# Kernel tuning notes

Hardware: AMD Instinct MI355X
Metric: run time of the kernel (lower is better)

The kernel has to match this reference:

```python
import math
import jax, jax.numpy as jnp
import numpy as np

LAMBDA_INIT = 0.8
GN_EPS = 1e-5

B, H, S, D = 2, 16, 2048, 128  # batch, heads, seq, head_dim


def setup_inputs() -> dict:
    key = jax.random.key(0)
    ks = jax.random.split(key, 8)
    return {
        "q": jax.random.normal(ks[0], (B, H, S, 2 * D), dtype=jnp.float32),
        "k": jax.random.normal(ks[1], (B, H, S, 2 * D), dtype=jnp.float32),
        "v": jax.random.normal(ks[2], (B, H, S, D), dtype=jnp.float32),
        "lam_q1": jax.random.normal(ks[3], (D,), dtype=jnp.float32),
        "lam_q2": jax.random.normal(ks[4], (D,), dtype=jnp.float32),
        "lam_k1": jax.random.normal(ks[5], (D,), dtype=jnp.float32),
        "lam_k2": jax.random.normal(ks[6], (D,), dtype=jnp.float32),
        "gn_weight": jnp.ones((H * D,), dtype=jnp.float32),
        "gn_bias": jnp.zeros((H * D,), dtype=jnp.float32),
    }


def reference(q, k, v, lam_q1, lam_q2, lam_k1, lam_k2, gn_weight, gn_bias):
    d = q.shape[-1] // 2
    scale = 1.0 / math.sqrt(d)
    Q1, Q2 = q[..., :d], q[..., d:]
    K1, K2 = k[..., :d], k[..., d:]
    # dual score matrices [B,H,S,S]
    w1 = jax.nn.softmax(jnp.einsum('bhsd,bhtd->bhst', Q1, K1) * scale, axis=-1)
    w2 = jax.nn.softmax(jnp.einsum('bhsd,bhtd->bhst', Q2, K2) * scale, axis=-1)
    lam = jnp.exp(jnp.dot(lam_q1, lam_k1)) - jnp.exp(jnp.dot(lam_q2, lam_k2)) + LAMBDA_INIT
    weights = w1 - lam * w2
    out = jnp.einsum('bhst,bhtd->bhsd', weights, v)  # [B,H,S,D]
    # GroupNorm(num_groups=H, num_channels=H*D) applied on [B, H*D, S]:
    # channel c = h*D + dd, normalization per (batch, head) over (D, S).
    mean = out.mean(axis=(2, 3), keepdims=True)
    var = out.var(axis=(2, 3), keepdims=True)
    normed = (out - mean) * jax.lax.rsqrt(var + GN_EPS)
    gamma = gn_weight.reshape(1, out.shape[1], 1, d)
    beta = gn_bias.reshape(1, out.shape[1], 1, d)
    return (normed * gamma + beta) * (1.0 - LAMBDA_INIT)
```

## Files before the change

### kernel.cpp

```cpp
#include <hip/hip_runtime.h>
#include <cstddef>

constexpr int B = 2, H = 16, S = 2048, D = 128;
constexpr int BH = B * H;
constexpr int TWOD = 2 * D;
constexpr int QTILE = 128;
constexpr int BC = 32;
constexpr int NKT = S / BC;
constexpr float SC2 = 0.08838834764831845f * 1.4426950408889634f;
constexpr float LAM_INIT = 0.8f;
constexpr float GN_EPS = 1e-5f;

typedef __attribute__((ext_vector_type(8))) short short8;
typedef __attribute__((ext_vector_type(4))) float f32x4;

__device__ __forceinline__ unsigned short f2b(float f) {
  unsigned int u = __float_as_uint(f);
  u += 0x7fffu + ((u >> 16) & 1u);
  return (unsigned short)(u >> 16);
}

__device__ __forceinline__ void async_copy16(const void* g, void* l) {
  typedef __attribute__((address_space(1))) const void gvoid;
  typedef __attribute__((address_space(3))) void lvoid;
  __builtin_amdgcn_global_load_lds((gvoid*)g, (lvoid*)l, 16, 0, 0);
}

__global__ void lam_kernel(const float* __restrict__ lq1, const float* __restrict__ lq2,
                           const float* __restrict__ lk1, const float* __restrict__ lk2,
                           float* __restrict__ wsf) {
  __shared__ float r1[128], r2[128];
  int t = threadIdx.x;
  r1[t] = lq1[t] * lk1[t];
  r2[t] = lq2[t] * lk2[t];
  __syncthreads();
  if (t == 0) {
    float s1 = 0.f, s2 = 0.f;
    for (int i = 0; i < 128; ++i) { s1 += r1[i]; s2 += r2[i]; }
    wsf[0] = expf(s1) - expf(s2) + LAM_INIT;
  }
}

__global__ void convk_kernel(const float* __restrict__ src, unsigned short* __restrict__ dst) {
  size_t i = ((size_t)blockIdx.x * 256 + threadIdx.x) * 8;
  float4 a = *(const float4*)(src + i);
  float4 b = *(const float4*)(src + i + 4);
  unsigned short u[8];
  u[0] = f2b(a.x); u[1] = f2b(a.y); u[2] = f2b(a.z); u[3] = f2b(a.w);
  u[4] = f2b(b.x); u[5] = f2b(b.y); u[6] = f2b(b.z); u[7] = f2b(b.w);
  *(uint4*)(dst + i) = *(uint4*)u;
}

__global__ void vt_kernel(const float* __restrict__ v, unsigned short* __restrict__ vtg) {
  __shared__ float tile[64][129];
  const int bh = blockIdx.y, s0 = blockIdx.x * 64, t = threadIdx.x;
#pragma unroll
  for (int i = 0; i < 8; ++i) {
    int idx = t + i * 256;
    int row = idx >> 5, c4 = idx & 31;
    float4 f = *(const float4*)(v + ((size_t)bh * S + s0 + row) * D + c4 * 4);
    tile[row][c4 * 4 + 0] = f.x; tile[row][c4 * 4 + 1] = f.y;
    tile[row][c4 * 4 + 2] = f.z; tile[row][c4 * 4 + 3] = f.w;
  }
  __syncthreads();
#pragma unroll
  for (int i = 0; i < 4; ++i) {
    int c = t + i * 256;
    int d = c >> 3, k8 = c & 7;
    unsigned short u[8];
#pragma unroll
    for (int j = 0; j < 8; ++j) u[j] = f2b(tile[k8 * 8 + j][d]);
    *(uint4*)(vtg + ((size_t)bh * D + d) * S + s0 + k8 * 8) = *(uint4*)u;
  }
}

__global__ __launch_bounds__(256, 2)
void attn_kernel(const float* __restrict__ q, const unsigned short* __restrict__ kbf,
                 const unsigned short* __restrict__ vtg,
                 float* __restrict__ wsf, float* __restrict__ out) {
  __shared__ __attribute__((aligned(16))) unsigned short Ks[2][32][256];
  __shared__ __attribute__((aligned(16))) unsigned short Vt[2][128][40];
  __shared__ __attribute__((aligned(16))) unsigned short Pa[4][2][32][40];
  __shared__ float sred[4][2];

  const int bh = blockIdx.x, qb = blockIdx.y;
  const int q0 = qb * QTILE;
  const int tid = threadIdx.x;
  const int wave = tid >> 6, lane = tid & 63;
  const int quad = lane >> 4, l16 = lane & 15;
  const float lam = wsf[0];

  short8 qf[2][2][4];
#pragma unroll
  for (int mt = 0; mt < 2; ++mt) {
    int qrow = q0 + wave * 32 + mt * 16 + l16;
    const float* qr = q + ((size_t)bh * S + qrow) * TWOD;
#pragma unroll
    for (int st = 0; st < 2; ++st)
#pragma unroll
      for (int ks = 0; ks < 4; ++ks) {
        const float* p = qr + st * D + ks * 32 + quad * 8;
        float4 f0 = *(const float4*)p;
        float4 f1 = *(const float4*)(p + 4);
        short8 v8;
        v8[0] = (short)f2b(f0.x); v8[1] = (short)f2b(f0.y);
        v8[2] = (short)f2b(f0.z); v8[3] = (short)f2b(f0.w);
        v8[4] = (short)f2b(f1.x); v8[5] = (short)f2b(f1.y);
        v8[6] = (short)f2b(f1.z); v8[7] = (short)f2b(f1.w);
        qf[mt][st][ks] = v8;
      }
  }

  const unsigned short* kbase = kbf + (size_t)bh * S * (size_t)TWOD;
  int goff[4];
#pragma unroll
  for (int i = 0; i < 4; ++i) {
    int L = i * 256 + tid;
    int row = L >> 5, cp = L & 31;
    int g = cp ^ (row & 7);
    goff[i] = row * 256 + g * 8;
  }
  const unsigned short* vbase = vtg + (size_t)bh * D * (size_t)S;
  const int vd0 = tid >> 2, vcp = tid & 3;

  f32x4 acc[2][2][8];
#pragma unroll
  for (int mt = 0; mt < 2; ++mt)
#pragma unroll
    for (int st = 0; st < 2; ++st)
#pragma unroll
      for (int n = 0; n < 8; ++n) acc[mt][st][n] = (f32x4){0.f, 0.f, 0.f, 0.f};
  float lacc[2][2][4];
#pragma unroll
  for (int mt = 0; mt < 2; ++mt)
#pragma unroll
    for (int st = 0; st < 2; ++st)
#pragma unroll
      for (int r = 0; r < 4; ++r) lacc[mt][st][r] = 0.f;

  const int pa_rd_off = (quad ^ ((l16 >> 2) & 3)) * 8;

  auto qk = [&](int st, int kb, f32x4 (&sa)[2][2]) {
#pragma unroll
    for (int nt = 0; nt < 2; ++nt) {
      const int row = nt * 16 + l16;
      const int rx = row & 7;
#pragma unroll
      for (int ks = 0; ks < 4; ++ks) {
        const int pos = (st * 16 + ks * 4 + quad) ^ rx;
        const short8 kf = *(const short8*)&Ks[kb][row][pos * 8];
        sa[0][nt] = __builtin_amdgcn_mfma_f32_16x16x32_bf16(qf[0][st][ks], kf, sa[0][nt], 0, 0, 0);
        sa[1][nt] = __builtin_amdgcn_mfma_f32_16x16x32_bf16(qf[1][st][ks], kf, sa[1][nt], 0, 0, 0);
      }
    }
  };
  auto pexp = [&](int st, f32x4 (&sa)[2][2]) {
#pragma unroll
    for (int mt = 0; mt < 2; ++mt)
#pragma unroll
      for (int nt = 0; nt < 2; ++nt)
#pragma unroll
        for (int r = 0; r < 4; ++r) {
          float p = __builtin_amdgcn_exp2f(sa[mt][nt][r] * SC2);
          lacc[mt][st][r] += p;
          int colp = (((nt * 2) + (l16 >> 3)) ^ quad) * 8 + (l16 & 7);
          Pa[wave][st][mt * 16 + quad * 4 + r][colp] = f2b(p);
        }
  };
  auto pv = [&](int st, const short8 (&paf)[2], const short8 (&vf)[8]) {
#pragma unroll
    for (int nt8 = 0; nt8 < 8; ++nt8)
#pragma unroll
      for (int mt = 0; mt < 2; ++mt)
        acc[mt][st][nt8] = __builtin_amdgcn_mfma_f32_16x16x32_bf16(paf[mt], vf[nt8], acc[mt][st][nt8], 0, 0, 0);
  };

  {
    const uint4 z = {0u, 0u, 0u, 0u};
    unsigned short* pz = &Pa[0][0][0][0];
    for (int i = tid; i < 1280; i += 256) *(uint4*)(pz + i * 8) = z;
    unsigned short* vz = &Vt[1][0][0];
    for (int i = tid; i < 640; i += 256) *(uint4*)(vz + i * 8) = z;
#pragma unroll
    for (int i = 0; i < 4; ++i)
      async_copy16(kbase + goff[i], &Ks[0][0][0] + (i * 256 + tid) * 8);
    uint4 v0 = *(const uint4*)(vbase + (size_t)vd0 * S + vcp * 8);
    uint4 v1 = *(const uint4*)(vbase + (size_t)(vd0 + 64) * S + vcp * 8);
    *(uint4*)&Vt[0][vd0][vcp * 8] = v0;
    *(uint4*)&Vt[0][vd0 + 64][vcp * 8] = v1;
  }
  __syncthreads();

  for (int t = 0; t < NKT; ++t) {
    const int kbuf = t & 1;
    const int pvbuf = kbuf ^ 1;

    short8 paf[2][2], vf[8];
#pragma unroll
    for (int st = 0; st < 2; ++st)
#pragma unroll
      for (int mt = 0; mt < 2; ++mt)
        paf[st][mt] = *(const short8*)&Pa[wave][st][mt * 16 + l16][pa_rd_off];
#pragma unroll
    for (int nt8 = 0; nt8 < 8; ++nt8)
      vf[nt8] = *(const short8*)&Vt[pvbuf][nt8 * 16 + l16][quad * 8];

    const bool pre = (t + 1 < NKT);
    uint4 vr0, vr1;
    if (pre) {
      const unsigned short* vp = vbase + (t + 1) * BC + vcp * 8;
      vr0 = *(const uint4*)(vp + (size_t)vd0 * S);
      vr1 = *(const uint4*)(vp + (size_t)(vd0 + 64) * S);
      const unsigned short* kp = kbase + (size_t)(t + 1) * BC * TWOD;
      unsigned short* ldsb = &Ks[pvbuf][0][0];
#pragma unroll
      for (int i = 0; i < 4; ++i)
        async_copy16(kp + goff[i], ldsb + (i * 256 + tid) * 8);
    }

    f32x4 sa0[2][2], sa1[2][2];
#pragma unroll
    for (int mt = 0; mt < 2; ++mt)
#pragma unroll
      for (int nt = 0; nt < 2; ++nt) {
        sa0[mt][nt] = (f32x4){0.f, 0.f, 0.f, 0.f};
        sa1[mt][nt] = (f32x4){0.f, 0.f, 0.f, 0.f};
      }
    qk(0, kbuf, sa0);
    pv(0, paf[0], vf);
    pexp(0, sa0);
    qk(1, kbuf, sa1);
    pv(1, paf[1], vf);
    pexp(1, sa1);

    __syncthreads();
    if (pre) {
      *(uint4*)&Vt[pvbuf][vd0][vcp * 8] = vr0;
      *(uint4*)&Vt[pvbuf][vd0 + 64][vcp * 8] = vr1;
    }
  }

  {
    short8 paf[2][2], vf[8];
#pragma unroll
    for (int st = 0; st < 2; ++st)
#pragma unroll
      for (int mt = 0; mt < 2; ++mt)
        paf[st][mt] = *(const short8*)&Pa[wave][st][mt * 16 + l16][pa_rd_off];
#pragma unroll
    for (int nt8 = 0; nt8 < 8; ++nt8)
      vf[nt8] = *(const short8*)&Vt[1][nt8 * 16 + l16][quad * 8];
    pv(0, paf[0], vf);
    pv(1, paf[1], vf);
  }

#pragma unroll
  for (int mt = 0; mt < 2; ++mt)
#pragma unroll
    for (int st = 0; st < 2; ++st)
#pragma unroll
      for (int r = 0; r < 4; ++r) {
        float v = lacc[mt][st][r];
        v += __shfl_xor(v, 1, 16);
        v += __shfl_xor(v, 2, 16);
        v += __shfl_xor(v, 4, 16);
        v += __shfl_xor(v, 8, 16);
        lacc[mt][st][r] = v;
      }

  float sum = 0.f, ssq = 0.f;
#pragma unroll
  for (int mt = 0; mt < 2; ++mt) {
    float i1[4], i2[4];
#pragma unroll
    for (int r = 0; r < 4; ++r) {
      i1[r] = 1.f / lacc[mt][0][r];
      i2[r] = lam / lacc[mt][1][r];
    }
#pragma unroll
    for (int nt8 = 0; nt8 < 8; ++nt8)
#pragma unroll
      for (int r = 0; r < 4; ++r) {
        float o = acc[mt][0][nt8][r] * i1[r] - acc[mt][1][nt8][r] * i2[r];
        int row = q0 + wave * 32 + mt * 16 + quad * 4 + r;
        out[((size_t)bh * S + row) * D + nt8 * 16 + l16] = o;
        sum += o; ssq += o * o;
      }
  }
#pragma unroll
  for (int off = 32; off >= 1; off >>= 1) {
    sum += __shfl_xor(sum, off, 64);
    ssq += __shfl_xor(ssq, off, 64);
  }
  if (lane == 0) { sred[wave][0] = sum; sred[wave][1] = ssq; }
  __syncthreads();
  if (tid == 0) {
    float s0 = sred[0][0] + sred[1][0] + sred[2][0] + sred[3][0];
    float s1 = sred[0][1] + sred[1][1] + sred[2][1] + sred[3][1];
    int idx = bh * 16 + qb;
    wsf[64 + idx * 2] = s0;
    wsf[64 + idx * 2 + 1] = s1;
  }
}

__global__ void gn_kernel(float* __restrict__ out, const float* __restrict__ gw,
                          const float* __restrict__ gb, const float* __restrict__ wsf) {
  const int bh = blockIdx.x, part = blockIdx.y;
  const int h = bh & (H - 1);
  float sum = 0.f, ssq = 0.f;
  for (int j = 0; j < 16; ++j) {
    sum += wsf[64 + (bh * 16 + j) * 2];
    ssq += wsf[64 + (bh * 16 + j) * 2 + 1];
  }
  const float invn = 1.f / (float)(S * D);
  const float mean = sum * invn;
  const float var = ssq * invn - mean * mean;
  const float rstd = rsqrtf(var + GN_EPS);
  const float outscale = 1.f - LAM_INIT;
  const float4* g4 = (const float4*)(gw + h * D);
  const float4* b4 = (const float4*)(gb + h * D);
  float4* o4 = (float4*)(out + (size_t)bh * S * D);
  const int chunks_per = (S * D / 4) / 8;
  const int c0 = part * chunks_per;
  for (int c = c0 + threadIdx.x; c < c0 + chunks_per; c += 256) {
    float4 vv = o4[c];
    int d4 = c & 31;
    float4 g = g4[d4], bb = b4[d4];
    vv.x = ((vv.x - mean) * rstd * g.x + bb.x) * outscale;
    vv.y = ((vv.y - mean) * rstd * g.y + bb.y) * outscale;
    vv.z = ((vv.z - mean) * rstd * g.z + bb.z) * outscale;
    vv.w = ((vv.w - mean) * rstd * g.w + bb.w) * outscale;
    o4[c] = vv;
  }
}

extern "C" void kernel_launch(void* const* d_in, const int* in_sizes, int n_in,
                              void* d_out, int out_size, void* d_ws, size_t ws_size,
                              hipStream_t stream) {
  (void)in_sizes; (void)n_in; (void)out_size; (void)ws_size;
  const float* q   = (const float*)d_in[0];
  const float* k   = (const float*)d_in[1];
  const float* v   = (const float*)d_in[2];
  const float* lq1 = (const float*)d_in[3];
  const float* lq2 = (const float*)d_in[4];
  const float* lk1 = (const float*)d_in[5];
  const float* lk2 = (const float*)d_in[6];
  const float* gw  = (const float*)d_in[7];
  const float* gb  = (const float*)d_in[8];
  float* out = (float*)d_out;
  float* wsf = (float*)d_ws;
  unsigned short* vtg = (unsigned short*)((char*)d_ws + 8192);
  unsigned short* kbf = (unsigned short*)((char*)d_ws + 8192 + (size_t)BH * D * S * 2);

  lam_kernel<<<dim3(1), dim3(128), 0, stream>>>(lq1, lq2, lk1, lk2, wsf);
  convk_kernel<<<dim3(BH * S * TWOD / 2048), dim3(256), 0, stream>>>(k, kbf);
  vt_kernel<<<dim3(S / 64, BH), dim3(256), 0, stream>>>(v, vtg);
  attn_kernel<<<dim3(BH, S / QTILE), dim3(256), 0, stream>>>(q, kbf, vtg, wsf, out);
  gn_kernel<<<dim3(BH, 8), dim3(256), 0, stream>>>(out, gw, gb, wsf);
}
```

Measured before the change: 400.6 us.

## Fuse lambda into K conversion, prescale Q, transpose QK MFMA for packed P stores

Folds the lambda computation into the K-to-bf16 conversion kernel using a wave shuffle reduction, which removes one kernel launch. Q is prescaled by the softmax scale when converted to bf16, so the per-element multiply before exp2 goes away. The QK MFMA operands are swapped so each lane holds four consecutive key columns of one query row. This lets P be written to LDS as packed 8-byte stores, and row sums need only two cross-quad shuffles instead of four. The trade-off is a Pa layout without the XOR swizzle, which may cause LDS bank conflicts, and slightly different bf16 rounding of Q.

```diff
diff --git a/kernel.cpp b/kernel.cpp
--- a/kernel.cpp
+++ b/kernel.cpp
@@ -26,22 +26,21 @@
   __builtin_amdgcn_global_load_lds((gvoid*)g, (lvoid*)l, 16, 0, 0);
 }
 
-__global__ void lam_kernel(const float* __restrict__ lq1, const float* __restrict__ lq2,
-                           const float* __restrict__ lk1, const float* __restrict__ lk2,
-                           float* __restrict__ wsf) {
-  __shared__ float r1[128], r2[128];
-  int t = threadIdx.x;
-  r1[t] = lq1[t] * lk1[t];
-  r2[t] = lq2[t] * lk2[t];
-  __syncthreads();
-  if (t == 0) {
-    float s1 = 0.f, s2 = 0.f;
-    for (int i = 0; i < 128; ++i) { s1 += r1[i]; s2 += r2[i]; }
-    wsf[0] = expf(s1) - expf(s2) + LAM_INIT;
-  }
-}
-
-__global__ void convk_kernel(const float* __restrict__ src, unsigned short* __restrict__ dst) {
+__global__ void convk_kernel(const float* __restrict__ src, unsigned short* __restrict__ dst,
+                             const float* __restrict__ lq1, const float* __restrict__ lq2,
+                             const float* __restrict__ lk1, const float* __restrict__ lk2,
+                             float* __restrict__ wsf) {
+  if (blockIdx.x == 0 && threadIdx.x < 64) {
+    int t = threadIdx.x;
+    float s1 = lq1[t] * lk1[t] + lq1[t + 64] * lk1[t + 64];
+    float s2 = lq2[t] * lk2[t] + lq2[t + 64] * lk2[t + 64];
+#pragma unroll
+    for (int off = 32; off >= 1; off >>= 1) {
+      s1 += __shfl_xor(s1, off, 64);
+      s2 += __shfl_xor(s2, off, 64);
+    }
+    if (t == 0) wsf[0] = expf(s1) - expf(s2) + LAM_INIT;
+  }
   size_t i = ((size_t)blockIdx.x * 256 + threadIdx.x) * 8;
   float4 a = *(const float4*)(src + i);
   float4 b = *(const float4*)(src + i + 4);
@@ -103,10 +102,10 @@
         float4 f0 = *(const float4*)p;
         float4 f1 = *(const float4*)(p + 4);
         short8 v8;
-        v8[0] = (short)f2b(f0.x); v8[1] = (short)f2b(f0.y);
-        v8[2] = (short)f2b(f0.z); v8[3] = (short)f2b(f0.w);
-        v8[4] = (short)f2b(f1.x); v8[5] = (short)f2b(f1.y);
-        v8[6] = (short)f2b(f1.z); v8[7] = (short)f2b(f1.w);
+        v8[0] = (short)f2b(f0.x * SC2); v8[1] = (short)f2b(f0.y * SC2);
+        v8[2] = (short)f2b(f0.z * SC2); v8[3] = (short)f2b(f0.w * SC2);
+        v8[4] = (short)f2b(f1.x * SC2); v8[5] = (short)f2b(f1.y * SC2);
+        v8[6] = (short)f2b(f1.z * SC2); v8[7] = (short)f2b(f1.w * SC2);
         qf[mt][st][ks] = v8;
       }
   }
@@ -130,15 +129,11 @@
     for (int st = 0; st < 2; ++st)
 #pragma unroll
       for (int n = 0; n < 8; ++n) acc[mt][st][n] = (f32x4){0.f, 0.f, 0.f, 0.f};
-  float lacc[2][2][4];
+  float lacc[2][2];
 #pragma unroll
   for (int mt = 0; mt < 2; ++mt)
 #pragma unroll
-    for (int st = 0; st < 2; ++st)
-#pragma unroll
-      for (int r = 0; r < 4; ++r) lacc[mt][st][r] = 0.f;
-
-  const int pa_rd_off = (quad ^ ((l16 >> 2) & 3)) * 8;
+    for (int st = 0; st < 2; ++st) lacc[mt][st] = 0.f;
 
   auto qk = [&](int st, int kb, f32x4 (&sa)[2][2]) {
 #pragma unroll
@@ -149,8 +144,8 @@
       for (int ks = 0; ks < 4; ++ks) {
         const int pos = (st * 16 + ks * 4 + quad) ^ rx;
         const short8 kf = *(const short8*)&Ks[kb][row][pos * 8];
-        sa[0][nt] = __builtin_amdgcn_mfma_f32_16x16x32_bf16(qf[0][st][ks], kf, sa[0][nt], 0, 0, 0);
-        sa[1][nt] = __builtin_amdgcn_mfma_f32_16x16x32_bf16(qf[1][st][ks], kf, sa[1][nt], 0, 0, 0);
+        sa[0][nt] = __builtin_amdgcn_mfma_f32_16x16x32_bf16(kf, qf[0][st][ks], sa[0][nt], 0, 0, 0);
+        sa[1][nt] = __builtin_amdgcn_mfma_f32_16x16x32_bf16(kf, qf[1][st][ks], sa[1][nt], 0, 0, 0);
       }
     }
   };
@@ -158,14 +153,17 @@
 #pragma unroll
     for (int mt = 0; mt < 2; ++mt)
 #pragma unroll
-      for (int nt = 0; nt < 2; ++nt)
-#pragma unroll
-        for (int r = 0; r < 4; ++r) {
-          float p = __builtin_amdgcn_exp2f(sa[mt][nt][r] * SC2);
-          lacc[mt][st][r] += p;
-          int colp = (((nt * 2) + (l16 >> 3)) ^ quad) * 8 + (l16 & 7);
-          Pa[wave][st][mt * 16 + quad * 4 + r][colp] = f2b(p);
-        }
+      for (int nt = 0; nt < 2; ++nt) {
+        float p0 = __builtin_amdgcn_exp2f(sa[mt][nt][0]);
+        float p1 = __builtin_amdgcn_exp2f(sa[mt][nt][1]);
+        float p2 = __builtin_amdgcn_exp2f(sa[mt][nt][2]);
+        float p3 = __builtin_amdgcn_exp2f(sa[mt][nt][3]);
+        lacc[mt][st] += (p0 + p1) + (p2 + p3);
+        uint2 w;
+        w.x = (unsigned int)f2b(p0) | ((unsigned int)f2b(p1) << 16);
+        w.y = (unsigned int)f2b(p2) | ((unsigned int)f2b(p3) << 16);
+        *(uint2*)&Pa[wave][st][mt * 16 + l16][nt * 16 + quad * 4] = w;
+      }
   };
   auto pv = [&](int st, const short8 (&paf)[2], const short8 (&vf)[8]) {
 #pragma unroll
@@ -200,7 +198,7 @@
     for (int st = 0; st < 2; ++st)
 #pragma unroll
       for (int mt = 0; mt < 2; ++mt)
-        paf[st][mt] = *(const short8*)&Pa[wave][st][mt * 16 + l16][pa_rd_off];
+        paf[st][mt] = *(const short8*)&Pa[wave][st][mt * 16 + l16][quad * 8];
 #pragma unroll
     for (int nt8 = 0; nt8 < 8; ++nt8)
       vf[nt8] = *(const short8*)&Vt[pvbuf][nt8 * 16 + l16][quad * 8];
@@ -246,7 +244,7 @@
     for (int st = 0; st < 2; ++st)
 #pragma unroll
       for (int mt = 0; mt < 2; ++mt)
-        paf[st][mt] = *(const short8*)&Pa[wave][st][mt * 16 + l16][pa_rd_off];
+        paf[st][mt] = *(const short8*)&Pa[wave][st][mt * 16 + l16][quad * 8];
 #pragma unroll
     for (int nt8 = 0; nt8 < 8; ++nt8)
       vf[nt8] = *(const short8*)&Vt[1][nt8 * 16 + l16][quad * 8];
@@ -257,16 +255,12 @@
 #pragma unroll
   for (int mt = 0; mt < 2; ++mt)
 #pragma unroll
-    for (int st = 0; st < 2; ++st)
-#pragma unroll
-      for (int r = 0; r < 4; ++r) {
-        float v = lacc[mt][st][r];
-        v += __shfl_xor(v, 1, 16);
-        v += __shfl_xor(v, 2, 16);
-        v += __shfl_xor(v, 4, 16);
-        v += __shfl_xor(v, 8, 16);
-        lacc[mt][st][r] = v;
-      }
+    for (int st = 0; st < 2; ++st) {
+      float v = lacc[mt][st];
+      v += __shfl_xor(v, 16, 64);
+      v += __shfl_xor(v, 32, 64);
+      lacc[mt][st] = v;
+    }
 
   float sum = 0.f, ssq = 0.f;
 #pragma unroll
@@ -274,8 +268,8 @@
     float i1[4], i2[4];
 #pragma unroll
     for (int r = 0; r < 4; ++r) {
-      i1[r] = 1.f / lacc[mt][0][r];
-      i2[r] = lam / lacc[mt][1][r];
+      i1[r] = 1.f / __shfl(lacc[mt][0], quad * 4 + r, 64);
+      i2[r] = lam / __shfl(lacc[mt][1], quad * 4 + r, 64);
     }
 #pragma unroll
     for (int nt8 = 0; nt8 < 8; ++nt8)
@@ -352,8 +346,7 @@
   unsigned short* vtg = (unsigned short*)((char*)d_ws + 8192);
   unsigned short* kbf = (unsigned short*)((char*)d_ws + 8192 + (size_t)BH * D * S * 2);
 
-  lam_kernel<<<dim3(1), dim3(128), 0, stream>>>(lq1, lq2, lk1, lk2, wsf);
-  convk_kernel<<<dim3(BH * S * TWOD / 2048), dim3(256), 0, stream>>>(k, kbf);
+  convk_kernel<<<dim3(BH * S * TWOD / 2048), dim3(256), 0, stream>>>(k, kbf, lq1, lq2, lk1, lk2, wsf);
   vt_kernel<<<dim3(S / 64, BH), dim3(256), 0, stream>>>(v, vtg);
   attn_kernel<<<dim3(BH, S / QTILE), dim3(256), 0, stream>>>(q, kbf, vtg, wsf, out);
   gn_kernel<<<dim3(BH, 8), dim3(256), 0, stream>>>(out, gw, gb, wsf);
```

After: 385.6 us. 1.04x faster.
